# Performance work log

Measured on AMD Instinct MI355X. Metric: run time of the kernel, lower is better.

## Reference

```python
import math
import jax, jax.numpy as jnp
import numpy as np

H = 8      # num_heads
K = 3      # polynomial order
WH, WW = 8, 8  # win_size


def _relative_position_index(wh, ww):
    coords = np.stack(np.meshgrid(np.arange(wh), np.arange(ww), indexing='ij'))  # [2,wh,ww]
    cf = coords.reshape(2, -1)                       # [2, N]
    rel = cf[:, :, None] - cf[:, None, :]            # [2, N, N]
    rel = rel.transpose(1, 2, 0).astype(np.int64)    # [N, N, 2]
    rel[..., 0] += wh - 1
    rel[..., 1] += ww - 1
    rel[..., 0] *= 2 * ww - 1
    return rel.sum(-1)                               # [N, N]


def setup_inputs() -> dict:
    key = jax.random.key(0)
    ks = jax.random.split(key, 10)
    B, N, C = 1024, WH * WW, 256
    hd = C // H
    s = 0.02
    inp = {
        'x': jax.random.normal(ks[0], (B, N, C), dtype=jnp.float32),
        'Wq': jax.random.normal(ks[1], (C, C), dtype=jnp.float32) * s,
        'bq': jnp.zeros((C,), dtype=jnp.float32),
        'Wkv': jax.random.normal(ks[2], (C, 2 * C), dtype=jnp.float32) * s,
        'bkv': jnp.zeros((2 * C,), dtype=jnp.float32),
        'Wgate': jax.random.normal(ks[3], (hd, K + 1), dtype=jnp.float32) * s,
        'bgate': jnp.zeros((K + 1,), dtype=jnp.float32),
        'Wproj': jax.random.normal(ks[4], (C, C), dtype=jnp.float32) * s,
        'bproj': jnp.zeros((C,), dtype=jnp.float32),
        'bias_table': jax.random.normal(ks[5], ((2 * WH - 1) * (2 * WW - 1), H), dtype=jnp.float32) * s,
        'rel_index': jnp.asarray(_relative_position_index(WH, WW)),
    }
    return inp


def reference(x, Wq, bq, Wkv, bkv, Wgate, bgate, Wproj, bproj, bias_table, rel_index):
    B, N, C = x.shape
    hd = C // H
    # per-(batch,head) sigmoid gates over the K+1 polynomial orders
    gate = jax.nn.sigmoid(x.mean(axis=1).reshape(B, H, hd) @ Wgate + bgate)  # [B,H,K+1]
    gate = gate[..., None, None]                                             # [B,H,K+1,1,1]

    q = (x @ Wq + bq).reshape(B, N, H, hd).transpose(0, 2, 1, 3)             # [B,H,N,hd]
    kv = (x @ Wkv + bkv).reshape(B, N, 2, H, hd).transpose(2, 0, 3, 1, 4)
    k, v = kv[0], kv[1]                                                      # [B,H,N,hd]

    q = jax.nn.softmax(q, axis=-1)
    k = jax.nn.softmax(k, axis=-1)
    attn = jnp.einsum('bhnd,bhmd->bhnm', q, k)                               # [B,H,N,N] (>=0)

    bias = bias_table[rel_index.reshape(-1)].reshape(N, N, H).transpose(2, 0, 1)  # [H,N,N]
    attn = attn + jax.nn.relu(bias)[None]
    attn = (attn + attn.transpose(0, 1, 3, 2)) * 0.5

    # symmetric degree normalization: D^{-1/2} A D^{-1/2}, zero-degree rows untouched
    d = attn.sum(axis=-1)                                                    # [B,H,N]
    dn = jnp.where(d > 0, 1.0 / jnp.sqrt(jnp.where(d > 0, d, 1.0)), d)
    attn = attn * dn[:, :, None, :] * dn[:, :, :, None]

    I = jnp.eye(N, dtype=attn.dtype)
    L = I - attn        # Laplacian
    L_hat = I + attn    # 2I - L

    # tmp[i] = L_hat^i (tmp[0] = I broadcasts)
    tmp = [I]
    E = I
    for _ in range(K):
        E = E @ L_hat
        tmp.append(E)

    c = [math.comb(K, j) / 2 ** K for j in range(K + 1)]
    out = c[0] * gate[:, :, K] * (tmp[K] @ v)                                # [B,H,N,hd]
    E = I
    for j in range(K):
        E = E @ L
        out = out + c[j + 1] * gate[:, :, j] * (E @ (tmp[K - j - 1] @ v))

    out = out.transpose(0, 2, 1, 3).reshape(B, N, C)
    out = out @ Wproj + bproj
    return out
```

## Files before the change

### kernel.cpp

```cpp
#include <hip/hip_runtime.h>
#include <hip/hip_bf16.h>

typedef __attribute__((ext_vector_type(8))) short bf16x8;
typedef __attribute__((ext_vector_type(4))) float f32x4;

__device__ __forceinline__ unsigned short f2bf(float f) {
    union { __hip_bfloat16 h; unsigned short u; } c;
    c.h = __float2bfloat16(f);
    return c.u;
}
__device__ __forceinline__ unsigned int pk2(float lo, float hi) {
    return (unsigned int)f2bf(lo) | ((unsigned int)f2bf(hi) << 16);
}
__device__ __forceinline__ bf16x8 as_bf(uint4 u) {
    union { uint4 a; bf16x8 b; } c; c.a = u; return c.b;
}
__device__ __forceinline__ float bf2f(unsigned short us) {
    return __uint_as_float(((unsigned int)us) << 16);
}
__device__ __forceinline__ void gload_lds16(const void* g, void* l) {
    __builtin_amdgcn_global_load_lds(
        (const __attribute__((address_space(1))) void*)g,
        (__attribute__((address_space(3))) void*)l, 16, 0, 0);
}

__global__ __launch_bounds__(256) void prep_kernel(
    const float* __restrict__ x,
    const float* __restrict__ Wq, const float* __restrict__ Wkv, const float* __restrict__ Wproj,
    const float* __restrict__ Wgate, const float* __restrict__ bgate,
    const float* __restrict__ bias_table, const int* __restrict__ rel_index,
    unsigned short* __restrict__ xbf, int use_xbf,
    unsigned short* __restrict__ wq, unsigned short* __restrict__ wk,
    unsigned short* __restrict__ wv, unsigned short* __restrict__ wp,
    float* __restrict__ bsym, float* __restrict__ wpoly)
{
    const int bid = blockIdx.x, t = threadIdx.x;
    if (bid < 1024) {
        __shared__ float mean_s[256];
        __shared__ float gsig[32];
        const float* xb = x + (size_t)bid * 16384;
        float s = 0.f;
        if (use_xbf) {
            unsigned short* xo = xbf + (size_t)bid * 16384;
            #pragma unroll 4
            for (int n = 0; n < 64; n++) { float v = xb[n * 256 + t]; s += v; xo[n * 256 + t] = f2bf(v); }
        } else {
            #pragma unroll 8
            for (int n = 0; n < 64; n++) s += xb[n * 256 + t];
        }
        mean_s[t] = s * (1.f / 64.f);
        __syncthreads();
        if (t < 32) {
            int h = t >> 2, j = t & 3;
            float g = bgate[j];
            #pragma unroll 8
            for (int dd = 0; dd < 32; dd++) g = fmaf(mean_s[h * 32 + dd], Wgate[dd * 4 + j], g);
            gsig[t] = 1.f / (1.f + __expf(-g));
        }
        __syncthreads();
        if (t < 8) {
            float g0 = gsig[t * 4], g1 = gsig[t * 4 + 1], g2 = gsig[t * 4 + 2], g3 = gsig[t * 4 + 3];
            float a = 0.125f * g3, bb = 0.375f * g0, cc = 0.375f * g1, dd = 0.125f * g2;
            float4 o;
            o.x = a + bb + cc + dd;
            o.y = 3.f * a + bb - cc - 3.f * dd;
            o.z = 3.f * a - bb - cc + 3.f * dd;
            o.w = a - bb + cc - dd;
            ((float4*)wpoly)[bid * 8 + t] = o;
        }
    } else if (bid < 2048) {
        int e = (bid - 1024) * 256 + t;
        int m = e >> 16, r = e & 65535, o = r >> 8, kk = r & 255;
        float v; unsigned short* dst;
        if (m == 0)      { v = Wq[kk * 256 + o];        dst = wq; }
        else if (m == 1) { v = Wkv[kk * 512 + o];       dst = wk; }
        else if (m == 2) { v = Wkv[kk * 512 + 256 + o]; dst = wv; }
        else             { v = Wproj[kk * 256 + o];     dst = wp; }
        dst[o * 256 + kk] = f2bf(v);
    } else {
        int e = (bid - 2048) * 256 + t;
        int hh = e >> 12, ij = e & 4095;
        int i = ij >> 6, j = ij & 63;
        float bij = bias_table[rel_index[ij] * 8 + hh];
        float bji = bias_table[rel_index[j * 64 + i] * 8 + hh];
        bsym[hh * 4096 + ij] = 0.5f * (fmaxf(bij, 0.f) + fmaxf(bji, 0.f));
    }
}

template <bool XBF>
__global__ __launch_bounds__(256, 4) void attn_kernel(
    const float* __restrict__ x, const unsigned short* __restrict__ xbf,
    const float* __restrict__ bq, const float* __restrict__ bkv,
    const unsigned short* __restrict__ wq, const unsigned short* __restrict__ wk,
    const unsigned short* __restrict__ wv,
    const float* __restrict__ bsym, const float* __restrict__ wpoly,
    unsigned short* __restrict__ hid)
{
    __shared__ __align__(16) unsigned char tile[32768];
    float* dn = (float*)(tile + 28672);

    const int bid = blockIdx.x;
    const int xcd = bid & 7, idx = bid >> 3;
    const int b = xcd * 128 + (idx >> 3), h = idx & 7;
    const int t = threadIdx.x;
    const int l = t & 63, w = t >> 6;
    const int lr = l & 15, qg = l >> 4;

    const float4 wv4 = ((const float4*)wpoly)[b * 8 + h];

    const int role = w;
    uint4 Bfr0[8], Bfr1[8];
    {
        const unsigned short* wsel = (role == 0) ? wq : (role == 1) ? wk : wv;
        const uint4* Wp = (const uint4*)wsel;
        const int ct0 = (role < 2) ? 0 : (role - 2);
        const int o0 = h * 32 + ct0 * 16 + lr;
        #pragma unroll
        for (int ks = 0; ks < 8; ks++) Bfr0[ks] = Wp[o0 * 32 + ks * 4 + qg];
        if (role < 2) {
            #pragma unroll
            for (int ks = 0; ks < 8; ks++) Bfr1[ks] = Wp[(o0 + 16) * 32 + ks * 4 + qg];
        }
    }

    if (XBF) {
        const unsigned short* xb = xbf + (size_t)b * 16384;
        const int rp = l >> 5, u = l & 31;
        #pragma unroll
        for (int i = 0; i < 8; i++) {
            int row = i * 8 + w * 2 + rp;
            int csrc = (u & 24) | ((u & 7) ^ (row & 7));
            gload_lds16(xb + row * 256 + csrc * 8, tile + (i * 8 + w * 2) * 512);
        }
    } else {
        const float* xb = x + (size_t)b * 16384;
        #pragma unroll
        for (int i = 0; i < 8; i++) {
            int e = t + i * 256;
            int row = e >> 5, c = e & 31;
            const float4* p = (const float4*)(xb + row * 256 + c * 8);
            float4 f0 = p[0], f1 = p[1];
            uint4 u;
            u.x = pk2(f0.x, f0.y); u.y = pk2(f0.z, f0.w);
            u.z = pk2(f1.x, f1.y); u.w = pk2(f1.z, f1.w);
            *(uint4*)(tile + row * 512 + ((c >> 3) << 7) + (((c & 7) ^ (row & 7)) << 4)) = u;
        }
    }

    f32x4 acc0[4], acc1[4];
    {
        const int ct0 = (role < 2) ? 0 : (role - 2);
        const int o0 = h * 32 + ct0 * 16 + lr;
        float b0 = (role == 0) ? bq[o0] : (role == 1) ? bkv[o0] : bkv[256 + o0];
        float b1 = (role == 0) ? bq[o0 + 16] : (role == 1) ? bkv[o0 + 16] : 0.f;
        #pragma unroll
        for (int mt = 0; mt < 4; mt++) {
            f32x4 z0 = {b0, b0, b0, b0}; acc0[mt] = z0;
            f32x4 z1 = {b1, b1, b1, b1}; acc1[mt] = z1;
        }
    }
    __syncthreads();

    __builtin_amdgcn_s_setprio(1);
    if (role < 2) {
        #pragma unroll
        for (int mt = 0; mt < 4; mt++) {
            const int rowA = mt * 16 + lr;
            #pragma unroll
            for (int ks = 0; ks < 8; ks++) {
                const int c = ks * 4 + qg;
                bf16x8 af = *(const bf16x8*)(tile + rowA * 512 + ((c >> 3) << 7) + (((c & 7) ^ (rowA & 7)) << 4));
                acc0[mt] = __builtin_amdgcn_mfma_f32_16x16x32_bf16(af, as_bf(Bfr0[ks]), acc0[mt], 0, 0, 0);
                acc1[mt] = __builtin_amdgcn_mfma_f32_16x16x32_bf16(af, as_bf(Bfr1[ks]), acc1[mt], 0, 0, 0);
            }
        }
    } else {
        #pragma unroll
        for (int mt = 0; mt < 4; mt++) {
            const int rowA = mt * 16 + lr;
            #pragma unroll
            for (int ks = 0; ks < 8; ks++) {
                const int c = ks * 4 + qg;
                bf16x8 af = *(const bf16x8*)(tile + rowA * 512 + ((c >> 3) << 7) + (((c & 7) ^ (rowA & 7)) << 4));
                acc0[mt] = __builtin_amdgcn_mfma_f32_16x16x32_bf16(af, as_bf(Bfr0[ks]), acc0[mt], 0, 0, 0);
            }
        }
    }
    __builtin_amdgcn_s_setprio(0);
    __syncthreads();

    float bsv[4][4];
    {
        const float* bh_ = bsym + h * 4096;
        #pragma unroll
        for (int jt = 0; jt < 4; jt++)
            #pragma unroll
            for (int r = 0; r < 4; r++)
                bsv[jt][r] = bh_[(w * 16 + qg * 4 + r) * 64 + jt * 16 + lr];
    }

    if (role < 2) {
        #pragma unroll
        for (int mt = 0; mt < 4; mt++)
            #pragma unroll
            for (int r = 0; r < 4; r++) {
                float e0 = __expf(acc0[mt][r]), e1 = __expf(acc1[mt][r]);
                float s = e0 + e1;
                s += __shfl_xor(s, 1); s += __shfl_xor(s, 2);
                s += __shfl_xor(s, 4); s += __shfl_xor(s, 8);
                float inv = 1.f / s;
                acc0[mt][r] = e0 * inv; acc1[mt][r] = e1 * inv;
            }
    }

    if (role == 0) {
        #pragma unroll
        for (int mt = 0; mt < 4; mt++)
            #pragma unroll
            for (int r = 0; r < 4; r++) {
                int row = mt * 16 + qg * 4 + r;
                int d0 = lr, d1 = 16 + lr;
                *(short*)(tile + row * 128 + (((d0 >> 3) ^ (row & 7)) << 4) + (d0 & 7) * 2) = (short)f2bf(acc0[mt][r]);
                *(short*)(tile + row * 128 + (((d1 >> 3) ^ (row & 7)) << 4) + (d1 & 7) * 2) = (short)f2bf(acc1[mt][r]);
            }
    } else if (role == 1) {
        #pragma unroll
        for (int mt = 0; mt < 4; mt++)
            #pragma unroll
            for (int r = 0; r < 4; r++) {
                int row = mt * 16 + qg * 4 + r;
                int d0 = lr, d1 = 16 + lr;
                *(short*)(tile + 8192 + row * 128 + (((d0 >> 3) ^ (row & 7)) << 4) + (d0 & 7) * 2) = (short)f2bf(acc0[mt][r]);
                *(short*)(tile + 8192 + row * 128 + (((d1 >> 3) ^ (row & 7)) << 4) + (d1 & 7) * 2) = (short)f2bf(acc1[mt][r]);
            }
    } else {
        const int d = (role - 2) * 16 + lr;
        #pragma unroll
        for (int mt = 0; mt < 4; mt++)
            #pragma unroll
            for (int r = 0; r < 4; r++) {
                int row = mt * 16 + qg * 4 + r;
                *(short*)(tile + 16384 + d * 128 + (((row >> 3) ^ (d & 7)) << 4) + (row & 7) * 2) = (short)f2bf(acc0[mt][r]);
            }
    }
    __syncthreads();

    float sv[4][4];
    float dnv[4];
    {
        const int swz = (qg ^ (lr & 7)) << 4;
        bf16x8 aqf = *(const bf16x8*)(tile + (w * 16 + lr) * 128 + swz);
        bf16x8 akf = *(const bf16x8*)(tile + 8192 + (w * 16 + lr) * 128 + swz);
        float rs[4] = {0.f, 0.f, 0.f, 0.f};
        __builtin_amdgcn_s_setprio(1);
        #pragma unroll
        for (int jt = 0; jt < 4; jt++) {
            bf16x8 bqf = *(const bf16x8*)(tile + (jt * 16 + lr) * 128 + swz);
            bf16x8 bkf = *(const bf16x8*)(tile + 8192 + (jt * 16 + lr) * 128 + swz);
            f32x4 qk = {0.f, 0.f, 0.f, 0.f}, kq = {0.f, 0.f, 0.f, 0.f};
            qk = __builtin_amdgcn_mfma_f32_16x16x32_bf16(aqf, bkf, qk, 0, 0, 0);
            kq = __builtin_amdgcn_mfma_f32_16x16x32_bf16(akf, bqf, kq, 0, 0, 0);
            #pragma unroll
            for (int r = 0; r < 4; r++) {
                float v = 0.5f * (qk[r] + kq[r]) + bsv[jt][r];
                sv[jt][r] = v;
                rs[r] += v;
            }
        }
        __builtin_amdgcn_s_setprio(0);
        #pragma unroll
        for (int r = 0; r < 4; r++) {
            float s = rs[r];
            s += __shfl_xor(s, 1); s += __shfl_xor(s, 2);
            s += __shfl_xor(s, 4); s += __shfl_xor(s, 8);
            dnv[r] = (s > 0.f) ? rsqrtf(s) : s;
        }
        if (lr == 0) {
            int base = w * 16 + qg * 4;
            dn[base + 0] = dnv[0]; dn[base + 1] = dnv[1];
            dn[base + 2] = dnv[2]; dn[base + 3] = dnv[3];
        }
    }
    __syncthreads();

    {
        float dnj[4];
        #pragma unroll
        for (int jt = 0; jt < 4; jt++) dnj[jt] = dn[jt * 16 + lr];
        #pragma unroll
        for (int jt = 0; jt < 4; jt++)
            #pragma unroll
            for (int r = 0; r < 4; r++) {
                int i = w * 16 + qg * 4 + r, j = jt * 16 + lr;
                *(short*)(tile + i * 128 + (((j >> 3) ^ (i & 7)) << 4) + (j & 7) * 2)
                    = (short)f2bf(sv[jt][r] * dnv[r] * dnj[jt]);
            }
    }
    __syncthreads();

    const float w0c = wv4.x, w1c = wv4.y, w2c = wv4.z, w3c = wv4.w;
    f32x4 y[2];
    #pragma unroll
    for (int ct = 0; ct < 2; ct++)
        #pragma unroll
        for (int r = 0; r < 4; r++) {
            int row = w * 16 + qg * 4 + r;
            int d = ct * 16 + lr;
            unsigned short us = *(unsigned short*)(tile + 16384 + d * 128 + (((row >> 3) ^ (d & 7)) << 4) + (row & 7) * 2);
            y[ct][r] = w0c * bf2f(us);
        }

#define AU_ROUND(SRC, DST, WC, WRITE) {                                                          \
    f32x4 u0 = {0.f,0.f,0.f,0.f}, u1 = {0.f,0.f,0.f,0.f};                                        \
    __builtin_amdgcn_s_setprio(1);                                                               \
    _Pragma("unroll")                                                                            \
    for (int ks2 = 0; ks2 < 2; ks2++) {                                                          \
        int c = ks2 * 4 + qg;                                                                    \
        bf16x8 af = *(const bf16x8*)(tile + (w * 16 + lr) * 128 + ((c ^ (lr & 7)) << 4));        \
        bf16x8 b0 = *(const bf16x8*)(tile + (SRC) + lr * 128 + ((c ^ (lr & 7)) << 4));           \
        bf16x8 b1 = *(const bf16x8*)(tile + (SRC) + (16 + lr) * 128 + ((c ^ (lr & 7)) << 4));    \
        u0 = __builtin_amdgcn_mfma_f32_16x16x32_bf16(af, b0, u0, 0, 0, 0);                       \
        u1 = __builtin_amdgcn_mfma_f32_16x16x32_bf16(af, b1, u1, 0, 0, 0);                       \
    }                                                                                            \
    __builtin_amdgcn_s_setprio(0);                                                               \
    y[0] += (WC) * u0; y[1] += (WC) * u1;                                                        \
    if (WRITE) {                                                                                 \
        _Pragma("unroll")                                                                        \
        for (int r = 0; r < 4; r++) {                                                            \
            int i = w * 16 + qg * 4 + r;                                                         \
            *(short*)(tile + (DST) + lr * 128 + (((i >> 3) ^ (lr & 7)) << 4) + (i & 7) * 2) = (short)f2bf(u0[r]); \
            *(short*)(tile + (DST) + (16 + lr) * 128 + (((i >> 3) ^ (lr & 7)) << 4) + (i & 7) * 2) = (short)f2bf(u1[r]); \
        }                                                                                        \
    }                                                                                            \
    __syncthreads();                                                                             \
}
    AU_ROUND(16384, 20480, w1c, 1)
    AU_ROUND(20480, 24576, w2c, 1)
    AU_ROUND(24576, 0,     w3c, 0)
#undef AU_ROUND

    #pragma unroll
    for (int ct = 0; ct < 2; ct++)
        #pragma unroll
        for (int r = 0; r < 4; r++) {
            int row = w * 16 + qg * 4 + r;
            int col = h * 32 + ct * 16 + lr;
            hid[((size_t)b * 64 + row) * 256 + col] = f2bf(y[ct][r]);
        }
}

__global__ __launch_bounds__(256) void proj_kernel(
    const unsigned short* __restrict__ hidden,
    const unsigned short* __restrict__ wp,
    const float* __restrict__ bproj,
    float* __restrict__ out)
{
    __shared__ __align__(16) unsigned char atile[65536];
    const int rb = blockIdx.x;
    const int t = threadIdx.x, l = t & 63, w = t >> 6;
    const int lr = l & 15, qg = l >> 4;

    const unsigned short* hb = hidden + (size_t)rb * 128 * 256;
    {
        const int rp = l >> 5, u = l & 31;
        #pragma unroll
        for (int i = 0; i < 16; i++) {
            int row = i * 8 + w * 2 + rp;
            int csrc = (u & 24) | ((u & 7) ^ (row & 7));
            gload_lds16(hb + row * 256 + csrc * 8, atile + (i * 8 + w * 2) * 512);
        }
    }
    float bzv[16];
    #pragma unroll
    for (int ct = 0; ct < 16; ct++) bzv[ct] = bproj[ct * 16 + lr];
    __syncthreads();

    bf16x8 af[2][8];
    #pragma unroll
    for (int rt = 0; rt < 2; rt++) {
        int row = w * 32 + rt * 16 + lr;
        #pragma unroll
        for (int ks = 0; ks < 8; ks++) {
            int c = ks * 4 + qg;
            af[rt][ks] = *(const bf16x8*)(atile + row * 512 + (((c & 24) | ((c & 7) ^ (row & 7))) << 4));
        }
    }

    const uint4* WP = (const uint4*)wp;
    #pragma unroll 2
    for (int ct = 0; ct < 16; ct++) {
        f32x4 a0 = {0.f, 0.f, 0.f, 0.f}, a1 = {0.f, 0.f, 0.f, 0.f};
        #pragma unroll
        for (int ks = 0; ks < 8; ks++) {
            bf16x8 bf = as_bf(WP[(ct * 16 + lr) * 32 + ks * 4 + qg]);
            a0 = __builtin_amdgcn_mfma_f32_16x16x32_bf16(af[0][ks], bf, a0, 0, 0, 0);
            a1 = __builtin_amdgcn_mfma_f32_16x16x32_bf16(af[1][ks], bf, a1, 0, 0, 0);
        }
        int colg = ct * 16 + lr;
        float bz = bzv[ct];
        #pragma unroll
        for (int r = 0; r < 4; r++) {
            int rowg = rb * 128 + w * 32 + qg * 4 + r;
            out[(size_t)rowg * 256 + colg] = a0[r] + bz;
            out[(size_t)(rowg + 16) * 256 + colg] = a1[r] + bz;
        }
    }
}

extern "C" void kernel_launch(void* const* d_in, const int* in_sizes, int n_in,
                              void* d_out, int out_size, void* d_ws, size_t ws_size,
                              hipStream_t stream) {
    const float* x          = (const float*)d_in[0];
    const float* Wq         = (const float*)d_in[1];
    const float* bq         = (const float*)d_in[2];
    const float* Wkv        = (const float*)d_in[3];
    const float* bkv        = (const float*)d_in[4];
    const float* Wgate      = (const float*)d_in[5];
    const float* bgate      = (const float*)d_in[6];
    const float* Wproj      = (const float*)d_in[7];
    const float* bproj      = (const float*)d_in[8];
    const float* bias_table = (const float*)d_in[9];
    const int*   rel_index  = (const int*)d_in[10];
    float* out = (float*)d_out;
    unsigned char* wsb = (unsigned char*)d_ws;

    const size_t HID   = 0;
    const size_t WQo   = 33554432;
    const size_t WKo   = WQo + 131072;
    const size_t WVo   = WKo + 131072;
    const size_t WPo   = WVo + 131072;
    const size_t BIASo = WPo + 131072;
    const size_t WPOLY = BIASo + 131072;
    const size_t XBFo  = WPOLY + 131072;
    const int use_xbf  = (ws_size >= XBFo + 33554432ull) ? 1 : 0;

    unsigned short* hid = (unsigned short*)(wsb + HID);
    unsigned short* wq  = (unsigned short*)(wsb + WQo);
    unsigned short* wk  = (unsigned short*)(wsb + WKo);
    unsigned short* wv  = (unsigned short*)(wsb + WVo);
    unsigned short* wp  = (unsigned short*)(wsb + WPo);
    float* bsym  = (float*)(wsb + BIASo);
    float* wpoly = (float*)(wsb + WPOLY);
    unsigned short* xbf = (unsigned short*)(wsb + XBFo);

    prep_kernel<<<dim3(2176), dim3(256), 0, stream>>>(
        x, Wq, Wkv, Wproj, Wgate, bgate, bias_table, rel_index,
        xbf, use_xbf, wq, wk, wv, wp, bsym, wpoly);
    if (use_xbf)
        attn_kernel<true><<<dim3(8192), dim3(256), 0, stream>>>(
            x, xbf, bq, bkv, wq, wk, wv, bsym, wpoly, hid);
    else
        attn_kernel<false><<<dim3(8192), dim3(256), 0, stream>>>(
            x, xbf, bq, bkv, wq, wk, wv, bsym, wpoly, hid);
    proj_kernel<<<dim3(512), dim3(256), 0, stream>>>(hid, wp, bproj, out);
}
```

Measured before the change: 142.8 us.

## Compute A² in parallel to cut dependent matmul rounds from three to two

Replaces the three sequential A·u rounds with two phases. The first computes A·v and the squared matrix A² together, storing A² in LDS. The second computes A²·v and A²·(A·v) at the same time. This removes one barrier and shortens the serial dependency chain, at the cost of extra MFMA work for the 64x64 A² product and an additional bf16 rounding of A².

```diff
diff --git a/kernel.cpp b/kernel.cpp
--- a/kernel.cpp
+++ b/kernel.cpp
@@ -310,34 +310,70 @@
             y[ct][r] = w0c * bf2f(us);
         }
 
-#define AU_ROUND(SRC, DST, WC, WRITE) {                                                          \
-    f32x4 u0 = {0.f,0.f,0.f,0.f}, u1 = {0.f,0.f,0.f,0.f};                                        \
-    __builtin_amdgcn_s_setprio(1);                                                               \
-    _Pragma("unroll")                                                                            \
-    for (int ks2 = 0; ks2 < 2; ks2++) {                                                          \
-        int c = ks2 * 4 + qg;                                                                    \
-        bf16x8 af = *(const bf16x8*)(tile + (w * 16 + lr) * 128 + ((c ^ (lr & 7)) << 4));        \
-        bf16x8 b0 = *(const bf16x8*)(tile + (SRC) + lr * 128 + ((c ^ (lr & 7)) << 4));           \
-        bf16x8 b1 = *(const bf16x8*)(tile + (SRC) + (16 + lr) * 128 + ((c ^ (lr & 7)) << 4));    \
-        u0 = __builtin_amdgcn_mfma_f32_16x16x32_bf16(af, b0, u0, 0, 0, 0);                       \
-        u1 = __builtin_amdgcn_mfma_f32_16x16x32_bf16(af, b1, u1, 0, 0, 0);                       \
-    }                                                                                            \
-    __builtin_amdgcn_s_setprio(0);                                                               \
-    y[0] += (WC) * u0; y[1] += (WC) * u1;                                                        \
-    if (WRITE) {                                                                                 \
-        _Pragma("unroll")                                                                        \
-        for (int r = 0; r < 4; r++) {                                                            \
-            int i = w * 16 + qg * 4 + r;                                                         \
-            *(short*)(tile + (DST) + lr * 128 + (((i >> 3) ^ (lr & 7)) << 4) + (i & 7) * 2) = (short)f2bf(u0[r]); \
-            *(short*)(tile + (DST) + (16 + lr) * 128 + (((i >> 3) ^ (lr & 7)) << 4) + (i & 7) * 2) = (short)f2bf(u1[r]); \
-        }                                                                                        \
-    }                                                                                            \
-    __syncthreads();                                                                             \
-}
-    AU_ROUND(16384, 20480, w1c, 1)
-    AU_ROUND(20480, 24576, w2c, 1)
-    AU_ROUND(24576, 0,     w3c, 0)
-#undef AU_ROUND
+    {
+        f32x4 u1a = {0.f,0.f,0.f,0.f}, u1b = {0.f,0.f,0.f,0.f};
+        f32x4 sq[4];
+        #pragma unroll
+        for (int jt = 0; jt < 4; jt++) { f32x4 z = {0.f,0.f,0.f,0.f}; sq[jt] = z; }
+        __builtin_amdgcn_s_setprio(1);
+        #pragma unroll
+        for (int ks2 = 0; ks2 < 2; ks2++) {
+            int c = ks2 * 4 + qg;
+            int so = (c ^ (lr & 7)) << 4;
+            bf16x8 af = *(const bf16x8*)(tile + (w * 16 + lr) * 128 + so);
+            bf16x8 v0 = *(const bf16x8*)(tile + 16384 + lr * 128 + so);
+            bf16x8 v1 = *(const bf16x8*)(tile + 16384 + (16 + lr) * 128 + so);
+            u1a = __builtin_amdgcn_mfma_f32_16x16x32_bf16(af, v0, u1a, 0, 0, 0);
+            u1b = __builtin_amdgcn_mfma_f32_16x16x32_bf16(af, v1, u1b, 0, 0, 0);
+            bf16x8 b0 = *(const bf16x8*)(tile + lr * 128 + so);
+            bf16x8 b1 = *(const bf16x8*)(tile + (16 + lr) * 128 + so);
+            bf16x8 b2 = *(const bf16x8*)(tile + (32 + lr) * 128 + so);
+            bf16x8 b3 = *(const bf16x8*)(tile + (48 + lr) * 128 + so);
+            sq[0] = __builtin_amdgcn_mfma_f32_16x16x32_bf16(af, b0, sq[0], 0, 0, 0);
+            sq[1] = __builtin_amdgcn_mfma_f32_16x16x32_bf16(af, b1, sq[1], 0, 0, 0);
+            sq[2] = __builtin_amdgcn_mfma_f32_16x16x32_bf16(af, b2, sq[2], 0, 0, 0);
+            sq[3] = __builtin_amdgcn_mfma_f32_16x16x32_bf16(af, b3, sq[3], 0, 0, 0);
+        }
+        __builtin_amdgcn_s_setprio(0);
+        y[0] += w1c * u1a; y[1] += w1c * u1b;
+        #pragma unroll
+        for (int r = 0; r < 4; r++) {
+            int i = w * 16 + qg * 4 + r;
+            *(short*)(tile + 20480 + lr * 128 + (((i >> 3) ^ (lr & 7)) << 4) + (i & 7) * 2) = (short)f2bf(u1a[r]);
+            *(short*)(tile + 20480 + (16 + lr) * 128 + (((i >> 3) ^ (lr & 7)) << 4) + (i & 7) * 2) = (short)f2bf(u1b[r]);
+        }
+        #pragma unroll
+        for (int jt = 0; jt < 4; jt++)
+            #pragma unroll
+            for (int r = 0; r < 4; r++) {
+                int i = w * 16 + qg * 4 + r, j = jt * 16 + lr;
+                *(short*)(tile + 8192 + i * 128 + (((j >> 3) ^ (i & 7)) << 4) + (j & 7) * 2) = (short)f2bf(sq[jt][r]);
+            }
+    }
+    __syncthreads();
+
+    {
+        f32x4 u2a = {0.f,0.f,0.f,0.f}, u2b = {0.f,0.f,0.f,0.f};
+        f32x4 u3a = {0.f,0.f,0.f,0.f}, u3b = {0.f,0.f,0.f,0.f};
+        __builtin_amdgcn_s_setprio(1);
+        #pragma unroll
+        for (int ks2 = 0; ks2 < 2; ks2++) {
+            int c = ks2 * 4 + qg;
+            int so = (c ^ (lr & 7)) << 4;
+            bf16x8 af = *(const bf16x8*)(tile + 8192 + (w * 16 + lr) * 128 + so);
+            bf16x8 v0 = *(const bf16x8*)(tile + 16384 + lr * 128 + so);
+            bf16x8 v1 = *(const bf16x8*)(tile + 16384 + (16 + lr) * 128 + so);
+            bf16x8 a0 = *(const bf16x8*)(tile + 20480 + lr * 128 + so);
+            bf16x8 a1 = *(const bf16x8*)(tile + 20480 + (16 + lr) * 128 + so);
+            u2a = __builtin_amdgcn_mfma_f32_16x16x32_bf16(af, v0, u2a, 0, 0, 0);
+            u2b = __builtin_amdgcn_mfma_f32_16x16x32_bf16(af, v1, u2b, 0, 0, 0);
+            u3a = __builtin_amdgcn_mfma_f32_16x16x32_bf16(af, a0, u3a, 0, 0, 0);
+            u3b = __builtin_amdgcn_mfma_f32_16x16x32_bf16(af, a1, u3b, 0, 0, 0);
+        }
+        __builtin_amdgcn_s_setprio(0);
+        y[0] += w2c * u2a + w3c * u3a;
+        y[1] += w2c * u2b + w3c * u3b;
+    }
 
     #pragma unroll
     for (int ct = 0; ct < 2; ct++)
```

After: 145.1 us. About the same (+1.6%).
